# Kernel optimization log

Measured on AMD Instinct MI355X. Metric: run time of the kernel, lower is better.

## Reference

```python
import jax, jax.numpy as jnp
import numpy as np

N, N_FEAT, F1, F2, F3, N_Z = 4096, 512, 256, 128, 64, 16
SLOPE = 0.2
NEG = -9e16


def _xavier(key, shape):
    std = (2.0 / (shape[0] + shape[1])) ** 0.5
    return jax.random.normal(key, shape, dtype=jnp.float32) * std


def setup_inputs() -> dict:
    key = jax.random.key(0)
    ks = jax.random.split(key, 20)
    x = jax.random.normal(ks[0], (N, N_FEAT), dtype=jnp.float32)
    adj = jax.random.randint(ks[1], (N, N), 0, 2, dtype=jnp.int32)
    dims = [N_FEAT, F1, F2, F3, N_Z, F3, F2, F1, N_FEAT]
    inp = {"x": x, "adj": adj}
    for i in range(8):
        fi, fo = dims[i], dims[i + 1]
        inp[f"w{i+1}"] = _xavier(ks[2 + 2 * i], (fi, fo))
        inp[f"a{i+1}"] = _xavier(ks[3 + 2 * i], (2 * fo, 1))
    return inp


def _gat(x, adj_pos, w, a):
    h = x @ w                               # [N, f_out]
    f = h.shape[1]
    src = h @ a[:f]                         # [N, 1]
    tgt = h @ a[f:]                         # [N, 1]
    e = jax.nn.leaky_relu(src + tgt.T, SLOPE)  # [N, N] broadcast score sum
    e = jnp.where(adj_pos, e, NEG)
    attn = jax.nn.softmax(e, axis=-1)
    return attn @ h                          # [N, f_out]


def reference(x, adj, w1, a1, w2, a2, w3, a3, w4, a4, w5, a5, w6, a6, w7, a7, w8, a8):
    adj_pos = adj > 0
    h1 = _gat(x, adj_pos, w1, a1)
    h2 = _gat(h1, adj_pos, w2, a2)
    h3 = _gat(h2, adj_pos, w3, a3)
    h4 = _gat(h3, adj_pos, w4, a4)
    h5 = _gat(h4, adj_pos, w5, a5)
    h6 = _gat(h5, adj_pos, w6, a6)
    h7 = _gat(h6, adj_pos, w7, a7)
    x_bar = _gat(h7, adj_pos, w8, a8)
    return (x_bar, h1, h2, h3, h4)
```

## Files before the change

kernel.cpp:

```cpp
#include <hip/hip_runtime.h>
#include <hip/hip_bf16.h>
#include <hip/hip_fp16.h>


#define NROWS 4096
#define TMC 12.0f

typedef __attribute__((ext_vector_type(8))) short v8s;
typedef __attribute__((ext_vector_type(8))) _Float16 v8h;
typedef __attribute__((ext_vector_type(2))) _Float16 h2v;
typedef __attribute__((ext_vector_type(4))) float v4f;

__device__ inline unsigned short f2bf(float x) {
  union { float f; unsigned u; } v; v.f = x;
  unsigned r = v.u + 0x7fffu + ((v.u >> 16) & 1u);
  return (unsigned short)(r >> 16);
}

__global__ void pack_adj(const int* __restrict__ adj, unsigned long long* __restrict__ bits) {
  int row = blockIdx.x;
  int lane = threadIdx.x & 63, wave = threadIdx.x >> 6;
  for (int w = wave; w < 64; w += 4) {
    unsigned long long m = __ballot(adj[(size_t)row * NROWS + w * 64 + lane] > 0);
    if (lane == 0) bits[row * 64 + w] = m;
  }
}

struct WTArgs { const float* src[8]; unsigned short* dst[8]; int K[8]; int F[8]; };
__global__ void transpose_w(WTArgs A) {
  int z = blockIdx.z;
  const float* in = A.src[z];
  unsigned short* out = A.dst[z];
  int R = A.K[z], C = A.F[z];
  __shared__ unsigned short tile[32][33];
  int c0 = blockIdx.x * 32, r0 = blockIdx.y * 32;
  if (c0 >= C || r0 >= R) return;
#pragma unroll
  for (int dy = 0; dy < 32; dy += 8) {
    int r = r0 + threadIdx.y + dy, c = c0 + threadIdx.x;
    if (r < R && c < C) tile[threadIdx.y + dy][threadIdx.x] = f2bf(in[(size_t)r * C + c]);
  }
  __syncthreads();
#pragma unroll
  for (int dy = 0; dy < 32; dy += 8) {
    int c = c0 + threadIdx.y + dy, r = r0 + threadIdx.x;
    if (r < R && c < C) out[(size_t)c * R + r] = tile[threadIdx.x][threadIdx.y + dy];
  }
}

__global__ __launch_bounds__(128) void gemm_xw(const float* __restrict__ A,
                                               const unsigned short* __restrict__ BT,
                                               float* __restrict__ C,
                                               unsigned short* __restrict__ HTt,
                                               int K, int Nf) {
  __shared__ unsigned short zone[64 * 36];
  int lane = threadIdx.x & 63, wave = threadIdx.x >> 6;
  int quad = lane >> 4, l16 = lane & 15;
  int row0 = blockIdx.x * 32 + wave * 16;
  int col0 = blockIdx.y * 64;
  int nf = Nf - col0; nf = nf > 64 ? 4 : (nf + 15) / 16;
  v4f acc[4] = {{0.f,0.f,0.f,0.f},{0.f,0.f,0.f,0.f},{0.f,0.f,0.f,0.f},{0.f,0.f,0.f,0.f}};
  for (int k0 = 0; k0 < K; k0 += 32) {
    int kk = k0 + quad * 8;
    v8s a = {0,0,0,0,0,0,0,0};
    if (kk < K) {
      float4 f0 = *(const float4*)(A + (size_t)(row0 + l16) * K + kk);
      float4 f1 = *(const float4*)(A + (size_t)(row0 + l16) * K + kk + 4);
      union { v8s s; __hip_bfloat162 h[4]; } ua;
      ua.h[0] = __float22bfloat162_rn(make_float2(f0.x, f0.y));
      ua.h[1] = __float22bfloat162_rn(make_float2(f0.z, f0.w));
      ua.h[2] = __float22bfloat162_rn(make_float2(f1.x, f1.y));
      ua.h[3] = __float22bfloat162_rn(make_float2(f1.z, f1.w));
      a = ua.s;
    }
    for (int t = 0; t < nf; t++) {
      v8s b = {0,0,0,0,0,0,0,0};
      if (kk < K) b = *(const v8s*)(BT + (size_t)(col0 + t * 16 + l16) * K + kk);
      acc[t] = __builtin_amdgcn_mfma_f32_16x16x32_bf16(a, b, acc[t], 0, 0, 0);
    }
  }
  for (int t = 0; t < nf; t++) {
#pragma unroll
    for (int r = 0; r < 4; r++) {
      float v = acc[t][r];
      C[(size_t)(row0 + quad * 4 + r) * Nf + col0 + t * 16 + l16] = v;
      union { _Float16 h; unsigned short s; } cv; cv.h = (_Float16)v;
      zone[(t * 16 + l16) * 36 + wave * 16 + quad * 4 + r] = cv.s;
    }
  }
  __syncthreads();
  unsigned* dst = (unsigned*)(HTt + (size_t)(blockIdx.x) * Nf * 32 + (size_t)col0 * 32);
  const unsigned* zsrc = (const unsigned*)zone;
  int total = nf * 256;
  for (int idx = threadIdx.x; idx < total; idx += 128) {
    int f = idx >> 4, jp = idx & 15;
    dst[idx] = zsrc[f * 18 + jp];
  }
}

__global__ void gemv_srctgt(const float* __restrict__ H, const float* __restrict__ a,
                            float* __restrict__ src, float* __restrict__ Ev,
                            float* __restrict__ Gv, unsigned short* __restrict__ Ev16,
                            unsigned short* __restrict__ Gv16, int f) {
  int row = blockIdx.x * 4 + (threadIdx.x >> 6);
  int lane = threadIdx.x & 63;
  float s = 0.f, t = 0.f;
  for (int k = lane; k < f; k += 64) {
    float h = H[(size_t)row * f + k];
    s += h * a[k];
    t += h * a[f + k];
  }
#pragma unroll
  for (int off = 32; off; off >>= 1) { s += __shfl_down(s, off); t += __shfl_down(t, off); }
  if (lane == 0) {
    src[row] = s;
    float ev = __expf(t - TMC), gv = __expf(0.2f * (t - TMC));
    Ev[row] = ev; Gv[row] = gv;
    union { _Float16 h; unsigned short u; } ce, cg;
    ce.h = (_Float16)(ev * 16384.f);
    cg.h = (_Float16)(gv * 16.f);
    Ev16[row] = ce.u;
    Gv16[row] = cg.u;
  }
}

__global__ void pass1b(const unsigned long long* __restrict__ bits, const float* __restrict__ src,
                       const float* __restrict__ Ev, const float* __restrict__ Gv,
                       float* __restrict__ Av, float* __restrict__ Bv) {
  int row = blockIdx.x * 4 + (threadIdx.x >> 6);
  int lane = threadIdx.x & 63;
  float sp = src[row] + TMC;
  float m = sp > 0.f ? sp : 0.2f * sp;
  float P = __expf(sp - m), Q = __expf(0.2f * sp - m);
  const unsigned long long* brow = bits + (size_t)row * 64;
  float lsum = 0.f;
  for (int k = 0; k < 64; k++) {
    unsigned long long w = brow[k];
    float v = fmaxf(P * Ev[k * 64 + lane], Q * Gv[k * 64 + lane]);
    lsum += ((w >> lane) & 1ull) ? v : 0.f;
  }
#pragma unroll
  for (int off = 32; off; off >>= 1) lsum += __shfl_xor(lsum, off);
  if (lane == 0) {
    float inv = 1.0f / lsum;
    Av[row] = P * inv;
    Bv[row] = Q * inv;
  }
}

template<int NF>
__global__ __launch_bounds__(256) void pass2f(const unsigned* __restrict__ adjW,
                                              const float* __restrict__ Av,
                                              const float* __restrict__ Bv,
                                              const unsigned short* __restrict__ Ev16,
                                              const unsigned short* __restrict__ Gv16,
                                              const unsigned short* __restrict__ HTt,
                                              float* __restrict__ out,
                                              float* __restrict__ part, int F, int js) {
  const int W = NF * 16, Wp = W + 4;
  __shared__ float zone[32 * Wp];
  int lane = threadIdx.x & 63, wave = threadIdx.x >> 6;
  int quad = lane >> 4, l16 = lane & 15;
  int i0 = blockIdx.x * 32;
  int fc0 = blockIdx.y * W;
  const size_t F32 = (size_t)F * 32;
  int jrange = NROWS / js;
  int jlen = jrange / 4;
  int jstart = blockIdx.z * jrange + wave * jlen;

  h2v Ai2[2], Bi2[2];
  const unsigned* arow[2];
#pragma unroll
  for (int ni = 0; ni < 2; ni++) {
    int i = i0 + ni * 16 + l16;
    _Float16 ai = (_Float16)(Av[i] * 0x1p-14f);
    _Float16 bi = (_Float16)(Bv[i] * 0x1p-4f);
    Ai2[ni] = (h2v){ai, ai};
    Bi2[ni] = (h2v){bi, bi};
    arow[ni] = adjW + (size_t)i * 128;
  }
  v4f acc[2][NF];
#pragma unroll
  for (int ni = 0; ni < 2; ni++)
#pragma unroll
    for (int t = 0; t < NF; t++) acc[ni][t] = (v4f){0.f, 0.f, 0.f, 0.f};

  for (int j0 = jstart; j0 < jstart + jlen; j0 += 128) {
    uint4 aw[2];
    aw[0] = *(const uint4*)(arow[0] + (j0 >> 5));
    aw[1] = *(const uint4*)(arow[1] + (j0 >> 5));
    unsigned awa[2][4] = {{aw[0].x, aw[0].y, aw[0].z, aw[0].w},
                          {aw[1].x, aw[1].y, aw[1].z, aw[1].w}};
#pragma unroll
    for (int u = 0; u < 4; u++) {
      int ju = j0 + u * 32;
      int jb = ju + quad * 8;
      union { v8s s; h2v h2[4]; } ue, ug;
      ue.s = *(const v8s*)(Ev16 + jb);
      ug.s = *(const v8s*)(Gv16 + jb);
      const unsigned short* bp =
          HTt + (size_t)(ju >> 5) * F32 + (size_t)(fc0 + l16) * 32 + quad * 8;
      union { v8s s; v8h h; } bfr[NF];
#pragma unroll
      for (int t = 0; t < NF; t++) bfr[t].s = *(const v8s*)(bp + t * 512);
#pragma unroll
      for (int ni = 0; ni < 2; ni++) {
        unsigned bb = awa[ni][u] >> (quad * 8);
        union { v8h h; unsigned u32[4]; } ua;
#pragma unroll
        for (int p = 0; p < 4; p++) {
          h2v w2 = __builtin_elementwise_max(Ai2[ni] * ue.h2[p], Bi2[ni] * ug.h2[p]);
          unsigned msk = (((bb >> (2 * p)) & 1u) ? 0x0000FFFFu : 0u)
                       | (((bb >> (2 * p + 1)) & 1u) ? 0xFFFF0000u : 0u);
          union { h2v h2; unsigned u; } tw; tw.h2 = w2;
          ua.u32[p] = tw.u & msk;
        }
#pragma unroll
        for (int t = 0; t < NF; t++)
          acc[ni][t] = __builtin_amdgcn_mfma_f32_16x16x32_f16(ua.h, bfr[t].h, acc[ni][t], 0, 0, 0);
      }
    }
  }

  for (int w = 0; w < 4; w++) {
    if (wave == w) {
#pragma unroll
      for (int ni = 0; ni < 2; ni++)
#pragma unroll
        for (int t = 0; t < NF; t++)
#pragma unroll
          for (int r = 0; r < 4; r++) {
            int idx = (ni * 16 + quad * 4 + r) * Wp + t * 16 + l16;
            if (w == 0) zone[idx] = acc[ni][t][r];
            else        zone[idx] += acc[ni][t][r];
          }
    }
    __syncthreads();
  }
  float* dst = (blockIdx.z == 0) ? out : part + (size_t)(blockIdx.z - 1) * NROWS * F;
  for (int idx = threadIdx.x; idx < 32 * W; idx += 256) {
    int rrow = idx / W, ccol = idx - rrow * W;
    dst[(size_t)(i0 + rrow) * F + fc0 + ccol] = zone[rrow * Wp + ccol];
  }
}

__global__ void reduce_add(const float* __restrict__ part, float* __restrict__ out, int n,
                           int nslab) {
  int i = blockIdx.x * 256 + threadIdx.x;
  if (i < n) {
    float s = out[i];
    for (int z = 0; z < nslab; z++) s += part[(size_t)z * n + i];
    out[i] = s;
  }
}

static void launch_pass2(int NF, dim3 grid, const unsigned* adjW, const float* Av, const float* Bv,
                         const unsigned short* Ev16, const unsigned short* Gv16,
                         const unsigned short* HTt, float* out, float* part, int F, int js,
                         hipStream_t stream) {
  switch (NF) {
    case 8: pass2f<8><<<grid, 256, 0, stream>>>(adjW, Av, Bv, Ev16, Gv16, HTt, out, part, F, js);
            break;
    case 4: pass2f<4><<<grid, 256, 0, stream>>>(adjW, Av, Bv, Ev16, Gv16, HTt, out, part, F, js);
            break;
    default: pass2f<1><<<grid, 256, 0, stream>>>(adjW, Av, Bv, Ev16, Gv16, HTt, out, part, F, js);
            break;
  }
}

extern "C" void kernel_launch(void* const* d_in, const int* in_sizes, int n_in,
                              void* d_out, int out_size, void* d_ws, size_t ws_size,
                              hipStream_t stream) {
  static const int fin[8]  = {512, 256, 128, 64, 16, 64, 128, 256};
  static const int fout[8] = {256, 128, 64, 16, 64, 128, 256, 512};

  const float* x = (const float*)d_in[0];
  const int* adj = (const int*)d_in[1];
  char* ws = (char*)d_ws;
  unsigned long long* bits = (unsigned long long*)(ws);
  unsigned short* WTall = (unsigned short*)(ws + (2u << 20));
  float* H            = (float*)(ws + (6u << 20));
  unsigned short* HTt = (unsigned short*)(ws + (14u << 20));
  float* srcv  = (float*)(ws + (19u << 20));
  float* Av    = (float*)(ws + (19u << 20) + 49152);
  float* Bv    = (float*)(ws + (19u << 20) + 65536);
  float* Ev    = (float*)(ws + (19u << 20) + 81920);
  float* Gv    = (float*)(ws + (19u << 20) + 98304);
  unsigned short* Ev16 = (unsigned short*)(ws + (19u << 20) + 114688);
  unsigned short* Gv16 = (unsigned short*)(ws + (19u << 20) + 122880);
  float* o5    = (float*)(ws + (20u << 20));
  float* o6    = (float*)(ws + (21u << 20));
  float* o7    = (float*)(ws + (23u << 20));
  float* part = H;

  float* outp = (float*)d_out;
  float* xbar = outp;
  float* h1 = outp + (size_t)NROWS * 512;
  float* h2 = h1 + (size_t)NROWS * 256;
  float* h3 = h2 + (size_t)NROWS * 128;
  float* h4 = h3 + (size_t)NROWS * 64;

  float* louts[8] = {h1, h2, h3, h4, o5, o6, o7, xbar};
  const float* lins[8] = {x, h1, h2, h3, h4, o5, o6, o7};

  unsigned short* WT[8];
  { size_t off = 0;
    for (int t = 0; t < 8; t++) { WT[t] = WTall + off; off += (size_t)fin[t] * fout[t]; } }

  pack_adj<<<dim3(4096), dim3(256), 0, stream>>>(adj, bits);

  WTArgs wa;
  for (int t = 0; t < 8; t++) {
    wa.src[t] = (const float*)d_in[2 + 2 * t];
    wa.dst[t] = WT[t];
    wa.K[t] = fin[t];
    wa.F[t] = fout[t];
  }
  transpose_w<<<dim3(16, 16, 8), dim3(32, 8), 0, stream>>>(wa);

  for (int t = 0; t < 8; t++) {
    int K = fin[t], F = fout[t];
    const float* At = (const float*)d_in[3 + 2 * t];
    const float* Xin = lins[t];
    float* Ot = louts[t];

    int NF = F >= 128 ? 8 : (F >= 64 ? 4 : 1);
    int fc = F / (16 * NF);
    int js = (F == 512) ? 1 : (F == 256 ? 2 : 4);

    gemm_xw<<<dim3(128, (F + 63) / 64), dim3(128), 0, stream>>>(Xin, WT[t], H, HTt, K, F);
    gemv_srctgt<<<dim3(1024), dim3(256), 0, stream>>>(H, At, srcv, Ev, Gv, Ev16, Gv16, F);
    pass1b<<<dim3(1024), dim3(256), 0, stream>>>(bits, srcv, Ev, Gv, Av, Bv);
    launch_pass2(NF, dim3(128, fc, js), (const unsigned*)bits, Av, Bv, Ev16, Gv16, HTt, Ot, part,
                 F, js, stream);
    if (js > 1)
      reduce_add<<<dim3((NROWS * F + 255) / 256), dim3(256), 0, stream>>>(part, Ot, NROWS * F,
                                                                          js - 1);
  }
}
```

Before: 533.3 us.

## Fuse softmax denominator into pass2 via ones-column MFMA, drop pass1b kernel

Removes the separate pass1b kernel that computed per-row softmax normalisers. The row sums are now accumulated inside pass2 with an extra MFMA against a vector of ones, and the division happens in the epilogue or in reduce_add when the j-range is split. This drops one launch and a full adjacency-bitmask scan per layer. In exchange it adds one MFMA per tile and sums the weights in fp16 inputs rather than fp32, which may change accuracy slightly.

```diff
diff --git a/kernel.cpp b/kernel.cpp
--- a/kernel.cpp
+++ b/kernel.cpp
@@ -99,8 +99,7 @@
 }
 
 __global__ void gemv_srctgt(const float* __restrict__ H, const float* __restrict__ a,
-                            float* __restrict__ src, float* __restrict__ Ev,
-                            float* __restrict__ Gv, unsigned short* __restrict__ Ev16,
+                            float* __restrict__ src, unsigned short* __restrict__ Ev16,
                             unsigned short* __restrict__ Gv16, int f) {
   int row = blockIdx.x * 4 + (threadIdx.x >> 6);
   int lane = threadIdx.x & 63;
@@ -114,49 +113,24 @@
   for (int off = 32; off; off >>= 1) { s += __shfl_down(s, off); t += __shfl_down(t, off); }
   if (lane == 0) {
     src[row] = s;
-    float ev = __expf(t - TMC), gv = __expf(0.2f * (t - TMC));
-    Ev[row] = ev; Gv[row] = gv;
     union { _Float16 h; unsigned short u; } ce, cg;
-    ce.h = (_Float16)(ev * 16384.f);
-    cg.h = (_Float16)(gv * 16.f);
+    ce.h = (_Float16)(__expf(t - TMC) * 16384.f);
+    cg.h = (_Float16)(__expf(0.2f * (t - TMC)) * 16.f);
     Ev16[row] = ce.u;
     Gv16[row] = cg.u;
   }
 }
 
-__global__ void pass1b(const unsigned long long* __restrict__ bits, const float* __restrict__ src,
-                       const float* __restrict__ Ev, const float* __restrict__ Gv,
-                       float* __restrict__ Av, float* __restrict__ Bv) {
-  int row = blockIdx.x * 4 + (threadIdx.x >> 6);
-  int lane = threadIdx.x & 63;
-  float sp = src[row] + TMC;
-  float m = sp > 0.f ? sp : 0.2f * sp;
-  float P = __expf(sp - m), Q = __expf(0.2f * sp - m);
-  const unsigned long long* brow = bits + (size_t)row * 64;
-  float lsum = 0.f;
-  for (int k = 0; k < 64; k++) {
-    unsigned long long w = brow[k];
-    float v = fmaxf(P * Ev[k * 64 + lane], Q * Gv[k * 64 + lane]);
-    lsum += ((w >> lane) & 1ull) ? v : 0.f;
-  }
-#pragma unroll
-  for (int off = 32; off; off >>= 1) lsum += __shfl_xor(lsum, off);
-  if (lane == 0) {
-    float inv = 1.0f / lsum;
-    Av[row] = P * inv;
-    Bv[row] = Q * inv;
-  }
-}
-
 template<int NF>
 __global__ __launch_bounds__(256) void pass2f(const unsigned* __restrict__ adjW,
-                                              const float* __restrict__ Av,
-                                              const float* __restrict__ Bv,
+                                              const float* __restrict__ src,
                                               const unsigned short* __restrict__ Ev16,
                                               const unsigned short* __restrict__ Gv16,
                                               const unsigned short* __restrict__ HTt,
                                               float* __restrict__ out,
-                                              float* __restrict__ part, int F, int js) {
+                                              float* __restrict__ part,
+                                              float* __restrict__ ls0,
+                                              float* __restrict__ part_ls, int F, int js) {
   const int W = NF * 16, Wp = W + 4;
   __shared__ float zone[32 * Wp];
   int lane = threadIdx.x & 63, wave = threadIdx.x >> 6;
@@ -173,17 +147,23 @@
 #pragma unroll
   for (int ni = 0; ni < 2; ni++) {
     int i = i0 + ni * 16 + l16;
-    _Float16 ai = (_Float16)(Av[i] * 0x1p-14f);
-    _Float16 bi = (_Float16)(Bv[i] * 0x1p-4f);
+    float sp = src[i] + TMC;
+    float m = sp > 0.f ? sp : 0.2f * sp;
+    _Float16 ai = (_Float16)(__expf(sp - m) * 0x1p-14f);
+    _Float16 bi = (_Float16)(__expf(0.2f * sp - m) * 0x1p-4f);
     Ai2[ni] = (h2v){ai, ai};
     Bi2[ni] = (h2v){bi, bi};
     arow[ni] = adjW + (size_t)i * 128;
   }
-  v4f acc[2][NF];
-#pragma unroll
-  for (int ni = 0; ni < 2; ni++)
+  const v8h ones = {(_Float16)1.f, (_Float16)1.f, (_Float16)1.f, (_Float16)1.f,
+                    (_Float16)1.f, (_Float16)1.f, (_Float16)1.f, (_Float16)1.f};
+  v4f acc[2][NF], accl[2];
+#pragma unroll
+  for (int ni = 0; ni < 2; ni++) {
+    accl[ni] = (v4f){0.f, 0.f, 0.f, 0.f};
 #pragma unroll
     for (int t = 0; t < NF; t++) acc[ni][t] = (v4f){0.f, 0.f, 0.f, 0.f};
+  }
 
   for (int j0 = jstart; j0 < jstart + jlen; j0 += 128) {
     uint4 aw[2];
@@ -218,6 +198,7 @@
 #pragma unroll
         for (int t = 0; t < NF; t++)
           acc[ni][t] = __builtin_amdgcn_mfma_f32_16x16x32_f16(ua.h, bfr[t].h, acc[ni][t], 0, 0, 0);
+        accl[ni] = __builtin_amdgcn_mfma_f32_16x16x32_f16(ua.h, ones, accl[ni], 0, 0, 0);
       }
     }
   }
@@ -225,7 +206,7 @@
   for (int w = 0; w < 4; w++) {
     if (wave == w) {
 #pragma unroll
-      for (int ni = 0; ni < 2; ni++)
+      for (int ni = 0; ni < 2; ni++) {
 #pragma unroll
         for (int t = 0; t < NF; t++)
 #pragma unroll
@@ -234,37 +215,65 @@
             if (w == 0) zone[idx] = acc[ni][t][r];
             else        zone[idx] += acc[ni][t][r];
           }
+        if (l16 == 0) {
+#pragma unroll
+          for (int r = 0; r < 4; r++) {
+            int idx = (ni * 16 + quad * 4 + r) * Wp + W;
+            if (w == 0) zone[idx] = accl[ni][r];
+            else        zone[idx] += accl[ni][r];
+          }
+        }
+      }
     }
     __syncthreads();
   }
-  float* dst = (blockIdx.z == 0) ? out : part + (size_t)(blockIdx.z - 1) * NROWS * F;
-  for (int idx = threadIdx.x; idx < 32 * W; idx += 256) {
-    int rrow = idx / W, ccol = idx - rrow * W;
-    dst[(size_t)(i0 + rrow) * F + fc0 + ccol] = zone[rrow * Wp + ccol];
-  }
-}
-
-__global__ void reduce_add(const float* __restrict__ part, float* __restrict__ out, int n,
+
+  if (js == 1) {
+    if (threadIdx.x < 32) zone[threadIdx.x * Wp + W] = 1.0f / zone[threadIdx.x * Wp + W];
+    __syncthreads();
+    for (int idx = threadIdx.x; idx < 32 * W; idx += 256) {
+      int rrow = idx / W, ccol = idx - rrow * W;
+      out[(size_t)(i0 + rrow) * F + fc0 + ccol] = zone[rrow * Wp + ccol] * zone[rrow * Wp + W];
+    }
+  } else {
+    float* dst = (blockIdx.z == 0) ? out : part + (size_t)(blockIdx.z - 1) * NROWS * F;
+    for (int idx = threadIdx.x; idx < 32 * W; idx += 256) {
+      int rrow = idx / W, ccol = idx - rrow * W;
+      dst[(size_t)(i0 + rrow) * F + fc0 + ccol] = zone[rrow * Wp + ccol];
+    }
+    if (threadIdx.x < 32) {
+      float l = zone[threadIdx.x * Wp + W];
+      if (blockIdx.z == 0) ls0[i0 + threadIdx.x] = l;
+      else part_ls[(size_t)(blockIdx.z - 1) * NROWS + i0 + threadIdx.x] = l;
+    }
+  }
+}
+
+__global__ void reduce_add(const float* __restrict__ part, const float* __restrict__ part_ls,
+                           const float* __restrict__ ls0, float* __restrict__ out, int n, int F,
                            int nslab) {
   int i = blockIdx.x * 256 + threadIdx.x;
   if (i < n) {
+    int row = i / F;
     float s = out[i];
+    float l = ls0[row];
     for (int z = 0; z < nslab; z++) s += part[(size_t)z * n + i];
-    out[i] = s;
-  }
-}
-
-static void launch_pass2(int NF, dim3 grid, const unsigned* adjW, const float* Av, const float* Bv,
+    for (int z = 0; z < nslab; z++) l += part_ls[(size_t)z * NROWS + row];
+    out[i] = s / l;
+  }
+}
+
+static void launch_pass2(int NF, dim3 grid, const unsigned* adjW, const float* src,
                          const unsigned short* Ev16, const unsigned short* Gv16,
-                         const unsigned short* HTt, float* out, float* part, int F, int js,
-                         hipStream_t stream) {
+                         const unsigned short* HTt, float* out, float* part, float* ls0,
+                         float* part_ls, int F, int js, hipStream_t stream) {
   switch (NF) {
-    case 8: pass2f<8><<<grid, 256, 0, stream>>>(adjW, Av, Bv, Ev16, Gv16, HTt, out, part, F, js);
-            break;
-    case 4: pass2f<4><<<grid, 256, 0, stream>>>(adjW, Av, Bv, Ev16, Gv16, HTt, out, part, F, js);
-            break;
-    default: pass2f<1><<<grid, 256, 0, stream>>>(adjW, Av, Bv, Ev16, Gv16, HTt, out, part, F, js);
-            break;
+    case 8: pass2f<8><<<grid, 256, 0, stream>>>(adjW, src, Ev16, Gv16, HTt, out, part, ls0,
+                                                part_ls, F, js); break;
+    case 4: pass2f<4><<<grid, 256, 0, stream>>>(adjW, src, Ev16, Gv16, HTt, out, part, ls0,
+                                                part_ls, F, js); break;
+    default: pass2f<1><<<grid, 256, 0, stream>>>(adjW, src, Ev16, Gv16, HTt, out, part, ls0,
+                                                 part_ls, F, js); break;
   }
 }
 
@@ -281,11 +290,9 @@
   unsigned short* WTall = (unsigned short*)(ws + (2u << 20));
   float* H            = (float*)(ws + (6u << 20));
   unsigned short* HTt = (unsigned short*)(ws + (14u << 20));
-  float* srcv  = (float*)(ws + (19u << 20));
-  float* Av    = (float*)(ws + (19u << 20) + 49152);
-  float* Bv    = (float*)(ws + (19u << 20) + 65536);
-  float* Ev    = (float*)(ws + (19u << 20) + 81920);
-  float* Gv    = (float*)(ws + (19u << 20) + 98304);
+  float* srcv    = (float*)(ws + (19u << 20));
+  float* ls0     = (float*)(ws + (19u << 20) + 49152);
+  float* part_ls = (float*)(ws + (19u << 20) + 65536);
   unsigned short* Ev16 = (unsigned short*)(ws + (19u << 20) + 114688);
   unsigned short* Gv16 = (unsigned short*)(ws + (19u << 20) + 122880);
   float* o5    = (float*)(ws + (20u << 20));
@@ -329,12 +336,11 @@
     int js = (F == 512) ? 1 : (F == 256 ? 2 : 4);
 
     gemm_xw<<<dim3(128, (F + 63) / 64), dim3(128), 0, stream>>>(Xin, WT[t], H, HTt, K, F);
-    gemv_srctgt<<<dim3(1024), dim3(256), 0, stream>>>(H, At, srcv, Ev, Gv, Ev16, Gv16, F);
-    pass1b<<<dim3(1024), dim3(256), 0, stream>>>(bits, srcv, Ev, Gv, Av, Bv);
-    launch_pass2(NF, dim3(128, fc, js), (const unsigned*)bits, Av, Bv, Ev16, Gv16, HTt, Ot, part,
-                 F, js, stream);
+    gemv_srctgt<<<dim3(1024), dim3(256), 0, stream>>>(H, At, srcv, Ev16, Gv16, F);
+    launch_pass2(NF, dim3(128, fc, js), (const unsigned*)bits, srcv, Ev16, Gv16, HTt, Ot, part,
+                 ls0, part_ls, F, js, stream);
     if (js > 1)
-      reduce_add<<<dim3((NROWS * F + 255) / 256), dim3(256), 0, stream>>>(part, Ot, NROWS * F,
-                                                                          js - 1);
-  }
-}
+      reduce_add<<<dim3((NROWS * F + 255) / 256), dim3(256), 0, stream>>>(part, part_ls, ls0, Ot,
+                                                                          NROWS * F, F, js - 1);
+  }
+}
```

After: 460.3 us. 13.7% less time.
